# Kernel tuning notes

Measured on AMD Instinct MI355X. Metric: run time of the kernel, lower is better.

The kernel has to match this reference:

```python
import jax, jax.numpy as jnp
import numpy as np

HOURS = 24 * 7  # 168
SU, SL, TU, TL = 100.0, 0.0, 1000.0, 0.0  # ex bounds
B, N, E = 32, 128, 64
NUM_USERS, NUM_LOCS = 10000, 100000


def setup_inputs() -> dict:
    key = jax.random.key(0)
    ks = jax.random.split(key, 10)
    traj = jax.random.randint(ks[0], (B, N, 3), 0, 10000, dtype=jnp.int32)
    # deltas in [0, 50], inside (SL,SU) and (TL,TU)
    mat = jax.random.uniform(ks[1], (B, N, N, 2), dtype=jnp.float32) * 50.0
    traj_len = jax.random.randint(ks[2], (B,), 1, N + 1, dtype=jnp.int32)
    s = 0.02
    emb_t = jax.random.normal(ks[3], (HOURS + 1, E), dtype=jnp.float32) * s
    emb_l = jax.random.normal(ks[4], (NUM_LOCS, E), dtype=jnp.float32) * s
    emb_u = jax.random.normal(ks[5], (NUM_USERS, E), dtype=jnp.float32) * s
    emb_su = jax.random.normal(ks[6], (2, E), dtype=jnp.float32) * s
    emb_sl = jax.random.normal(ks[7], (2, E), dtype=jnp.float32) * s
    emb_tu = jax.random.normal(ks[8], (2, E), dtype=jnp.float32) * s
    emb_tl = jax.random.normal(ks[9], (2, E), dtype=jnp.float32) * s
    return dict(traj=traj, mat=mat, traj_len=traj_len, emb_t=emb_t, emb_l=emb_l,
                emb_u=emb_u, emb_su=emb_su, emb_sl=emb_sl, emb_tu=emb_tu, emb_tl=emb_tl)


def reference(traj, mat, traj_len, emb_t, emb_l, emb_u, emb_su, emb_sl, emb_tu, emb_tl):
    # time-of-week bucketing: (t-1) % 168 + 1  ->  values in [1, 168]
    t_idx = (traj[:, :, 2] - 1) % HOURS + 1
    time = emb_t[t_idx]            # (B,N,E)
    loc = emb_l[traj[:, :, 1]]     # (B,N,E)
    user = emb_u[traj[:, :, 0]]    # (B,N,E)
    joint = time + loc + user

    delta_s = mat[:, :, :, 0]      # (B,N,N)
    delta_t = mat[:, :, :, 1]

    # vectorized replacement of the per-sample python loop: square 1-block of size traj_len[i]
    valid = jnp.arange(N)[None, :] < traj_len[:, None]          # (B,N) bool
    mask = (valid[:, :, None] & valid[:, None, :]).astype(jnp.int32)  # (B,N,N) in {0,1}

    esl, esu = emb_sl[mask], emb_su[mask]  # (B,N,N,E)
    etl, etu = emb_tl[mask], emb_tu[mask]

    vsl = (delta_s - SL)[..., None]
    vsu = (SU - delta_s)[..., None]
    vtl = (delta_t - TL)[..., None]
    vtu = (TU - delta_t)[..., None]

    space_interval = (esl * vsu + esu * vsl) / (SU - SL)
    time_interval = (etl * vtu + etu * vtl) / (TU - TL)
    delta = space_interval + time_interval  # (B,N,N,E)
    return joint, delta
```

## Files before the change

kernel.cpp:

```cpp
#include <hip/hip_runtime.h>


#define HOURS 168
#define BB 32
#define NN 128
#define EE 64
#define JOINT_ELEMS (BB * NN * EE)
#define JOINT4      (JOINT_ELEMS / 4)
#define DELTA4      (BB * NN * NN * EE / 4)
#define TOTAL4      (JOINT4 + DELTA4)

__device__ __forceinline__ float4 ld4(const float* p) {
    return *(const float4*)p;
}
__device__ __forceinline__ float4 f4add(float4 a, float4 b) {
    return make_float4(a.x + b.x, a.y + b.y, a.z + b.z, a.w + b.w);
}
__device__ __forceinline__ float4 f4sub(float4 a, float4 b) {
    return make_float4(a.x - b.x, a.y - b.y, a.z - b.z, a.w - b.w);
}
__device__ __forceinline__ float4 f4fma(float s, float4 a, float4 b) {
    return make_float4(fmaf(s, a.x, b.x), fmaf(s, a.y, b.y),
                       fmaf(s, a.z, b.z), fmaf(s, a.w, b.w));
}
__device__ __forceinline__ float4 f4sel(bool m, float4 a, float4 b) {
    return make_float4(m ? a.x : b.x, m ? a.y : b.y, m ? a.z : b.z, m ? a.w : b.w);
}

__global__ __launch_bounds__(256) void multiembed_kernel(
    const int*   __restrict__ traj,
    const float* __restrict__ mat,
    const int*   __restrict__ traj_len,
    const float* __restrict__ emb_t,
    const float* __restrict__ emb_l,
    const float* __restrict__ emb_u,
    const float* __restrict__ emb_su,
    const float* __restrict__ emb_sl,
    const float* __restrict__ emb_tu,
    const float* __restrict__ emb_tl,
    float*       __restrict__ out)
{
    const int tid    = blockIdx.x * blockDim.x + threadIdx.x;
    const int stride = gridDim.x * blockDim.x;
    const int e      = (tid & 15) * 4;

    const float4 sl0 = ld4(emb_sl + e),      sl1 = ld4(emb_sl + EE + e);
    const float4 su0 = ld4(emb_su + e),      su1 = ld4(emb_su + EE + e);
    const float4 tl0 = ld4(emb_tl + e),      tl1 = ld4(emb_tl + EE + e);
    const float4 tu0 = ld4(emb_tu + e),      tu1 = ld4(emb_tu + EE + e);

    const float4 base0 = f4add(sl0, tl0);
    const float4 base1 = f4add(sl1, tl1);
    const float4 d1_0  = f4sub(su0, sl0);
    const float4 d1_1  = f4sub(su1, sl1);
    const float4 d2_0  = f4sub(tu0, tl0);
    const float4 d2_1  = f4sub(tu1, tl1);

    float* const delta_out = out + JOINT_ELEMS;

    for (int q = tid; q < TOTAL4; q += stride) {
        if (q < JOINT4) {
            const int cell = q >> 4;
            const int u  = traj[cell * 3 + 0];
            const int l  = traj[cell * 3 + 1];
            const int t  = traj[cell * 3 + 2];
            int tm = (t - 1) % HOURS;
            if (tm < 0) tm += HOURS;
            tm += 1;
            float4 v = f4add(f4add(ld4(emb_t + tm * EE + e),
                                   ld4(emb_l + l  * EE + e)),
                             ld4(emb_u + u * EE + e));
            *(float4*)(out + q * 4) = v;
        } else {
            const int qd   = q - JOINT4;
            const int cell = qd >> 4;
            const int j    = cell & (NN - 1);
            const int i    = (cell >> 7) & (NN - 1);
            const int b    = cell >> 14;
            const int L    = traj_len[b];
            const bool m   = (i < L) && (j < L);

            const float2 dd = *(const float2*)(mat + (size_t)cell * 2);
            const float csu = dd.x * 0.01f;
            const float ctu = dd.y * 0.001f;

            float4 r = f4sel(m, base1, base0);
            r = f4fma(csu, f4sel(m, d1_1, d1_0), r);
            r = f4fma(ctu, f4sel(m, d2_1, d2_0), r);

            *(float4*)(delta_out + qd * 4) = r;
        }
    }
}

extern "C" void kernel_launch(void* const* d_in, const int* in_sizes, int n_in,
                              void* d_out, int out_size, void* d_ws, size_t ws_size,
                              hipStream_t stream) {
    const int*   traj     = (const int*)  d_in[0];
    const float* mat      = (const float*)d_in[1];
    const int*   traj_len = (const int*)  d_in[2];
    const float* emb_t    = (const float*)d_in[3];
    const float* emb_l    = (const float*)d_in[4];
    const float* emb_u    = (const float*)d_in[5];
    const float* emb_su   = (const float*)d_in[6];
    const float* emb_sl   = (const float*)d_in[7];
    const float* emb_tu   = (const float*)d_in[8];
    const float* emb_tl   = (const float*)d_in[9];
    float*       out      = (float*)d_out;

    multiembed_kernel<<<dim3(2048), dim3(256), 0, stream>>>(
        traj, mat, traj_len, emb_t, emb_l, emb_u,
        emb_su, emb_sl, emb_tu, emb_tl, out);
}
```

Measured before the change: 189.7 us.

## Split joint and delta work, use fixed-trip delta loop with nontemporal stores

Joint gather becomes a single guarded pass on the first threads, and the delta region is handled by a compile-time trip-count loop with strength-reduced pointers and a wave-uniform batch index. Per-iteration index decoding, the joint/delta branch and the per-element mask test on both i and j are removed. A max(i,j)<L test is used, with a ballot to pick uniform select paths. Outputs are written with nontemporal stores to reduce cache pollution on the large streaming write.

After: 176.6 us. 6.9% less time.

```diff
diff --git a/kernel.cpp b/kernel.cpp
--- a/kernel.cpp
+++ b/kernel.cpp
@@ -8,23 +8,14 @@
 #define JOINT_ELEMS (BB * NN * EE)
 #define JOINT4      (JOINT_ELEMS / 4)
 #define DELTA4      (BB * NN * NN * EE / 4)
-#define TOTAL4      (JOINT4 + DELTA4)
+#define NBLOCKS     2048
+#define NTHREADS    (NBLOCKS * 256)
+#define ITERS       (DELTA4 / NTHREADS)
 
-__device__ __forceinline__ float4 ld4(const float* p) {
-    return *(const float4*)p;
-}
-__device__ __forceinline__ float4 f4add(float4 a, float4 b) {
-    return make_float4(a.x + b.x, a.y + b.y, a.z + b.z, a.w + b.w);
-}
-__device__ __forceinline__ float4 f4sub(float4 a, float4 b) {
-    return make_float4(a.x - b.x, a.y - b.y, a.z - b.z, a.w - b.w);
-}
-__device__ __forceinline__ float4 f4fma(float s, float4 a, float4 b) {
-    return make_float4(fmaf(s, a.x, b.x), fmaf(s, a.y, b.y),
-                       fmaf(s, a.z, b.z), fmaf(s, a.w, b.w));
-}
-__device__ __forceinline__ float4 f4sel(bool m, float4 a, float4 b) {
-    return make_float4(m ? a.x : b.x, m ? a.y : b.y, m ? a.z : b.z, m ? a.w : b.w);
+typedef float f32x4 __attribute__((ext_vector_type(4)));
+
+__device__ __forceinline__ f32x4 ld4(const float* p) {
+    return *(const f32x4*)p;
 }
 
 __global__ __launch_bounds__(256) void multiembed_kernel(
@@ -40,56 +31,68 @@
     const float* __restrict__ emb_tl,
     float*       __restrict__ out)
 {
-    const int tid    = blockIdx.x * blockDim.x + threadIdx.x;
-    const int stride = gridDim.x * blockDim.x;
-    const int e      = (tid & 15) * 4;
+    const int tid = blockIdx.x * blockDim.x + threadIdx.x;
+    const int e   = (tid & 15) * 4;
 
-    const float4 sl0 = ld4(emb_sl + e),      sl1 = ld4(emb_sl + EE + e);
-    const float4 su0 = ld4(emb_su + e),      su1 = ld4(emb_su + EE + e);
-    const float4 tl0 = ld4(emb_tl + e),      tl1 = ld4(emb_tl + EE + e);
-    const float4 tu0 = ld4(emb_tu + e),      tu1 = ld4(emb_tu + EE + e);
+    const f32x4 sl0 = ld4(emb_sl + e), sl1 = ld4(emb_sl + EE + e);
+    const f32x4 su0 = ld4(emb_su + e), su1 = ld4(emb_su + EE + e);
+    const f32x4 tl0 = ld4(emb_tl + e), tl1 = ld4(emb_tl + EE + e);
+    const f32x4 tu0 = ld4(emb_tu + e), tu1 = ld4(emb_tu + EE + e);
 
-    const float4 base0 = f4add(sl0, tl0);
-    const float4 base1 = f4add(sl1, tl1);
-    const float4 d1_0  = f4sub(su0, sl0);
-    const float4 d1_1  = f4sub(su1, sl1);
-    const float4 d2_0  = f4sub(tu0, tl0);
-    const float4 d2_1  = f4sub(tu1, tl1);
+    const f32x4 base0 = sl0 + tl0, base1 = sl1 + tl1;
+    const f32x4 d1_0  = su0 - sl0, d1_1  = su1 - sl1;
+    const f32x4 d2_0  = tu0 - tl0, d2_1  = tu1 - tl1;
 
-    float* const delta_out = out + JOINT_ELEMS;
+    if (tid < JOINT4) {
+        const int cell = tid >> 4;
+        const int u = traj[cell * 3 + 0];
+        const int l = traj[cell * 3 + 1];
+        const int t = traj[cell * 3 + 2];
+        int tm = (t - 1) % HOURS;
+        if (tm < 0) tm += HOURS;
+        tm += 1;
+        f32x4 v = ld4(emb_t + tm * EE + e) + ld4(emb_l + (size_t)l * EE + e)
+                + ld4(emb_u + (size_t)u * EE + e);
+        __builtin_nontemporal_store(v, (f32x4*)(out + (size_t)tid * 4));
+    }
 
-    for (int q = tid; q < TOTAL4; q += stride) {
-        if (q < JOINT4) {
-            const int cell = q >> 4;
-            const int u  = traj[cell * 3 + 0];
-            const int l  = traj[cell * 3 + 1];
-            const int t  = traj[cell * 3 + 2];
-            int tm = (t - 1) % HOURS;
-            if (tm < 0) tm += HOURS;
-            tm += 1;
-            float4 v = f4add(f4add(ld4(emb_t + tm * EE + e),
-                                   ld4(emb_l + l  * EE + e)),
-                             ld4(emb_u + u * EE + e));
-            *(float4*)(out + q * 4) = v;
+    const int cell0 = tid >> 4;
+    const int j  = cell0 & (NN - 1);
+    const int i  = (cell0 >> 7) & (NN - 1);
+    const int mx = (i > j) ? i : j;
+    const int b0 = __builtin_amdgcn_readfirstlane(cell0 >> 14);
+
+    const float* mptr = mat + (size_t)cell0 * 2;
+    float*       dptr = out + JOINT_ELEMS + (size_t)tid * 4;
+
+    int b = b0;
+    #pragma unroll 4
+    for (int k = 0; k < ITERS; ++k) {
+        const int  L = traj_len[b];
+        const bool m = mx < L;
+
+        const float2 dd  = *(const float2*)mptr;
+        const float  csu = dd.x * 0.01f;
+        const float  ctu = dd.y * 0.001f;
+
+        f32x4 bse, v1, v2;
+        const unsigned long long bal = __ballot(m);
+        if (bal == 0xFFFFFFFFFFFFFFFFull) {
+            bse = base1; v1 = d1_1; v2 = d2_1;
+        } else if (bal == 0ull) {
+            bse = base0; v1 = d1_0; v2 = d2_0;
         } else {
-            const int qd   = q - JOINT4;
-            const int cell = qd >> 4;
-            const int j    = cell & (NN - 1);
-            const int i    = (cell >> 7) & (NN - 1);
-            const int b    = cell >> 14;
-            const int L    = traj_len[b];
-            const bool m   = (i < L) && (j < L);
+            bse = m ? base1 : base0;
+            v1  = m ? d1_1  : d1_0;
+            v2  = m ? d2_1  : d2_0;
+        }
 
-            const float2 dd = *(const float2*)(mat + (size_t)cell * 2);
-            const float csu = dd.x * 0.01f;
-            const float ctu = dd.y * 0.001f;
+        const f32x4 r = bse + csu * v1 + ctu * v2;
+        __builtin_nontemporal_store(r, (f32x4*)dptr);
 
-            float4 r = f4sel(m, base1, base0);
-            r = f4fma(csu, f4sel(m, d1_1, d1_0), r);
-            r = f4fma(ctu, f4sel(m, d2_1, d2_0), r);
-
-            *(float4*)(delta_out + qd * 4) = r;
-        }
+        b    += 2;
+        mptr += 32768 * 2;
+        dptr += (size_t)NTHREADS * 4;
     }
 }
 
@@ -108,7 +111,7 @@
     const float* emb_tl   = (const float*)d_in[9];
     float*       out      = (float*)d_out;
 
-    multiembed_kernel<<<dim3(2048), dim3(256), 0, stream>>>(
+    multiembed_kernel<<<dim3(NBLOCKS), dim3(256), 0, stream>>>(
         traj, mat, traj_len, emb_t, emb_l, emb_u,
         emb_su, emb_sl, emb_tu, emb_tl, out);
 }
```
